# Performance work log

Measured on AMD Instinct MI355X. Metric: run time of the kernel, lower is better.

## Reference

```python
import jax, jax.numpy as jnp
import numpy as np

EPS = 1e-20
TEMP = 0.07
HEAD_DIM = 128


def setup_inputs() -> dict:
    key = jax.random.key(0)
    k1, k2, k3 = jax.random.split(key, 3)
    B, C, T, H, W = 4, 512, 8, 32, 32
    x = jax.random.normal(k1, (B, C, T, H, W), dtype=jnp.float32)
    W_head = jax.random.normal(k2, (C, HEAD_DIM), dtype=jnp.float32) / np.sqrt(C).astype(np.float32)
    b_head = jax.random.normal(k3, (HEAD_DIM,), dtype=jnp.float32) * 0.01
    return {"x": x, "W_head": W_head, "b_head": b_head}


def _forward(x, W_head, b_head):
    B, C, T, H, W = x.shape
    N = H * W
    # linear head over channel dim (equivalent to permute->Linear->permute)
    feats = jnp.einsum('bcthw,cd->bdthw', x, W_head) + b_head[None, :, None, None, None]
    keys = feats.reshape(B, HEAD_DIM, T, N)
    # F.normalize(p=2, dim=1): x / max(||x||, 1e-12)
    norm = jnp.maximum(jnp.linalg.norm(keys, axis=1, keepdims=True), 1e-12)
    keys = keys / norm
    # affinity between consecutive frames: [B, T-1, N, N]
    A = jnp.einsum('bctn,bctm->btnm', keys[:, :, :-1], keys[:, :, 1:])
    A12 = jax.nn.softmax(A / TEMP, axis=-1)                         # forward stochastic mats
    A21 = jax.nn.softmax(jnp.swapaxes(A, -1, -2) / TEMP, axis=-1)   # backward stochastic mats
    A12s = jnp.swapaxes(A12, 0, 1)  # [T-1, B, N, N]
    A21s = jnp.swapaxes(A21, 0, 1)  # [T-1, B, N, N]

    # prefix products P[i] = A12[0] @ A12[1] @ ... @ A12[i]
    def step_p(carry, a):
        c = carry @ a
        return c, c
    _, Ptail = jax.lax.scan(step_p, A12s[0], A12s[1:])
    P = jnp.concatenate([A12s[:1], Ptail], axis=0)  # [T-1, B, N, N]

    # suffix products S[i] = A21[i] @ A21[i-1] @ ... @ A21[0]
    def step_s(carry, a):
        c = a @ carry
        return c, c
    _, Stail = jax.lax.scan(step_s, A21s[0], A21s[1:])
    S = jnp.concatenate([A21s[:1], Stail], axis=0)  # [T-1, B, N, N]

    # cycle walks for i = 1..T-2: aar_i = P[i] @ S[i]
    aars = jnp.matmul(P[1:], S[1:])  # [T-2, B, N, N]
    logits = jnp.log(aars + EPS)
    # cross-entropy with identity targets: loss = logsumexp - logit[n, n]
    lse = jax.nn.logsumexp(logits, axis=-1)                  # [T-2, B, N]
    diag = jnp.diagonal(logits, axis1=-2, axis2=-1)          # [T-2, B, N]
    losses = jnp.mean(lse - diag, axis=(1, 2))               # [T-2]
    preds = jnp.argmax(logits, axis=-1)                      # [T-2, B, N]
    tgt = jnp.arange(N)[None, None, :]
    accs = jnp.mean((preds == tgt).astype(jnp.float32), axis=(1, 2))
    # original returns (loss_of_last_walk, diags); diags exposed as stacked arrays
    return losses[-1], losses, accs


def reference(x, W_head, b_head):
    return _forward(x, W_head, b_head)
```

## Files before the change

### kernel.cpp

```cpp
#include <hip/hip_runtime.h>
#include <cstdint>
#include <cstddef>

typedef unsigned short u16;
typedef unsigned long long u64;
using short8 = __attribute__((ext_vector_type(8))) short;
using f32x4  = __attribute__((ext_vector_type(4))) float;

#define KEXP 20.609929155556620f

__device__ __forceinline__ u16 f2bf(float f) {
  unsigned u = __float_as_uint(f);
  u += 0x7fffu + ((u >> 16) & 1u);
  return (u16)(u >> 16);
}
__device__ __forceinline__ float bf2f(u16 h) { return __uint_as_float(((unsigned)h) << 16); }

typedef const unsigned int GASu32 __attribute__((address_space(1)));
typedef unsigned int LASu32 __attribute__((address_space(3)));

__device__ __forceinline__ void gload16(const u16* src, u16* dstLds) {
  __builtin_amdgcn_global_load_lds((GASu32*)src, (LASu32*)dstLds, 16, 0, 0);
}

__global__ __launch_bounds__(256) void transpose_x(const float* __restrict__ x, u16* __restrict__ xT) {
  __shared__ float t[32][33];
  int b = blockIdx.z, c0 = blockIdx.y * 32, s0 = blockIdx.x * 32;
  int tid = threadIdx.x;
  int ci = tid >> 3, s4 = (tid & 7) * 4;
  float4 v = *(const float4*)(x + ((size_t)b * 512 + c0 + ci) * 8192 + s0 + s4);
  t[ci][s4 + 0] = v.x; t[ci][s4 + 1] = v.y; t[ci][s4 + 2] = v.z; t[ci][s4 + 3] = v.w;
  __syncthreads();
  int si = tid >> 3, c4 = (tid & 7) * 4;
  ushort4 o;
  o.x = f2bf(t[c4 + 0][si]); o.y = f2bf(t[c4 + 1][si]);
  o.z = f2bf(t[c4 + 2][si]); o.w = f2bf(t[c4 + 3][si]);
  *(ushort4*)(xT + ((size_t)b * 8192 + s0 + si) * 512 + c0 + c4) = o;
}

__global__ __launch_bounds__(256) void transpose_w(const float* __restrict__ W, u16* __restrict__ Wt) {
  int idx = blockIdx.x * 256 + threadIdx.x;
  int d = idx >> 9, c = idx & 511;
  Wt[idx] = (d < 128) ? f2bf(W[c * 128 + d]) : (u16)0;
}

__global__ __launch_bounds__(256) void normalize_keys(u16* __restrict__ keys) {
  int wv = threadIdx.x >> 6, lane = threadIdx.x & 63;
  int row = blockIdx.x * 4 + wv;
  unsigned* p = (unsigned*)(keys + (size_t)row * 128) + lane;
  unsigned v = *p;
  float a = bf2f((u16)(v & 0xffffu)), b = bf2f((u16)(v >> 16));
  float s = a * a + b * b;
  #pragma unroll
  for (int m = 1; m < 64; m <<= 1) s += __shfl_xor(s, m, 64);
  float sc = 1.f / fmaxf(sqrtf(s), 1e-12f);
  *p = (unsigned)f2bf(a * sc) | ((unsigned)f2bf(b * sc) << 16);
}

__global__ __launch_bounds__(256) void reduce_sums(const float* __restrict__ rsEP, const float* __restrict__ csEP,
                                                   float* __restrict__ rsumE, float* __restrict__ csumE) {
  int idx = blockIdx.x * 256 + threadIdx.x;
  if (idx < 28672) {
    int z = idx >> 10, r = idx & 1023;
    float s = 0.f;
    #pragma unroll
    for (int k = 0; k < 16; ++k) s += rsEP[(size_t)z * 16384 + k * 1024 + r];
    rsumE[z * 1024 + r] = s;
  } else {
    int b2 = idx - 28672;
    int z = b2 >> 10, c = b2 & 1023;
    float s = 0.f;
    #pragma unroll
    for (int k = 0; k < 8; ++k) s += csEP[(size_t)z * 8192 + k * 1024 + c];
    csumE[z * 1024 + c] = s;
  }
}

__global__ __launch_bounds__(256) void k3_t0(const u16* __restrict__ E, const float* __restrict__ rsum,
                                             const float* __restrict__ csum,
                                             u16* __restrict__ P0, u16* __restrict__ S0) {
  int b = blockIdx.z, r = blockIdx.x;
  int zE = b * 7;
  const u16* e = E + ((size_t)zE << 20) + (size_t)r * 1024;
  float rr = 1.f / rsum[zE * 1024 + r];
  int c = threadIdx.x * 4;
  ushort4 v = *(const ushort4*)(e + c);
  float4 cv = *(const float4*)(csum + zE * 1024 + c);
  ushort4 o1, o2;
  float v0 = bf2f(v.x), v1 = bf2f(v.y), v2 = bf2f(v.z), v3 = bf2f(v.w);
  o1.x = f2bf(v0 * rr); o1.y = f2bf(v1 * rr); o1.z = f2bf(v2 * rr); o1.w = f2bf(v3 * rr);
  o2.x = f2bf(v0 / cv.x); o2.y = f2bf(v1 / cv.y); o2.z = f2bf(v2 / cv.z); o2.w = f2bf(v3 / cv.w);
  size_t base = ((size_t)b << 20) + (size_t)r * 1024 + c;
  *(ushort4*)(P0 + base) = o1;
  *(ushort4*)(S0 + base) = o2;
}

__global__ __launch_bounds__(256) void k3_tr(const u16* __restrict__ E, const float* __restrict__ rsum,
                                             const float* __restrict__ csum,
                                             u16* __restrict__ Bp, u16* __restrict__ Bs) {
  __shared__ u16 t[64][66];
  int z = blockIdx.z; int b = z / 6, tt = z % 6 + 1;
  int zE = b * 7 + tt;
  int er0 = blockIdx.x * 64, ec0 = blockIdx.y * 64;
  const u16* e = E + ((size_t)zE << 20);
  int tid = threadIdx.x;
  int ri = tid >> 4, c4 = (tid & 15) * 4;
  #pragma unroll
  for (int p = 0; p < 4; ++p) {
    ushort4 v = *(const ushort4*)(e + (size_t)(er0 + ri + p * 16) * 1024 + ec0 + c4);
    t[ri + p * 16][c4 + 0] = v.x; t[ri + p * 16][c4 + 1] = v.y;
    t[ri + p * 16][c4 + 2] = v.z; t[ri + p * 16][c4 + 3] = v.w;
  }
  __syncthreads();
  size_t outBase = (size_t)(b * 6 + tt - 1) << 20;
  float ir0 = 1.f / rsum[zE * 1024 + er0 + c4 + 0];
  float ir1 = 1.f / rsum[zE * 1024 + er0 + c4 + 1];
  float ir2 = 1.f / rsum[zE * 1024 + er0 + c4 + 2];
  float ir3 = 1.f / rsum[zE * 1024 + er0 + c4 + 3];
  #pragma unroll
  for (int p = 0; p < 4; ++p) {
    int roL = ri + p * 16;
    int ro = ec0 + roL;
    float ic = 1.f / csum[zE * 1024 + ro];
    float v0 = bf2f(t[c4 + 0][roL]), v1 = bf2f(t[c4 + 1][roL]);
    float v2 = bf2f(t[c4 + 2][roL]), v3 = bf2f(t[c4 + 3][roL]);
    ushort4 op, os;
    op.x = f2bf(v0 * ir0); op.y = f2bf(v1 * ir1); op.z = f2bf(v2 * ir2); op.w = f2bf(v3 * ir3);
    os.x = f2bf(v0 * ic);  os.y = f2bf(v1 * ic);  os.z = f2bf(v2 * ic);  os.w = f2bf(v3 * ic);
    size_t off = outBase + (size_t)ro * 1024 + er0 + c4;
    *(ushort4*)(Bp + off) = op;
    *(ushort4*)(Bs + off) = os;
  }
}

struct GemmBatch { const u16* A[24]; const u16* B[24]; u16* C[8]; };
enum { M_HEAD = 0, M_EXP = 1, M_PLAIN = 2, M_AAR = 3 };

__device__ __forceinline__ int lds_off32(int r, int kbyte) {
  int rp = r >> 1;
  int sl = (((r & 1) << 2) | (kbyte >> 4)) ^ (rp & 7);
  return rp * 128 + sl * 16;
}

#define GEMM_BODY(T, FA, FB, NA, NB)                                                    \
  {                                                                                     \
    int t_ = (T);                                                                       \
    if (t_ + 1 < nt) {                                                                  \
      if (t_ + 2 < nt) asm volatile("s_waitcnt vmcnt(4)" ::: "memory");                 \
      else             asm volatile("s_waitcnt vmcnt(0)" ::: "memory");                 \
      __builtin_amdgcn_s_barrier();                                                     \
      __builtin_amdgcn_sched_barrier(0);                                                \
      _Pragma("unroll")                                                                 \
      for (int f = 0; f < 8; ++f) NA[f] = *(const short8*)((const char*)An + offA[f]);  \
      _Pragma("unroll")                                                                 \
      for (int f = 0; f < 4; ++f) NB[f] = *(const short8*)((const char*)Bn + offB[f]);  \
      if (t_ + 3 < nt) {                                                                \
        int k0_ = (t_ + 3) << 5;                                                        \
        gload16(sA0 + k0_, Ac + d0); gload16(sA1 + k0_, Ac + d1);                       \
        gload16(sB0 + k0_, Bc + d0); gload16(sB1 + k0_, Bc + d1);                       \
      }                                                                                 \
      asm volatile("s_waitcnt lgkmcnt(12)" ::: "memory");                               \
    } else {                                                                            \
      asm volatile("s_waitcnt lgkmcnt(0)" ::: "memory");                                \
    }                                                                                   \
    __builtin_amdgcn_sched_barrier(0);                                                  \
    __builtin_amdgcn_s_setprio(1);                                                      \
    _Pragma("unroll")                                                                   \
    for (int fa = 0; fa < 8; ++fa)                                                      \
      _Pragma("unroll")                                                                 \
      for (int fb = 0; fb < 4; ++fb)                                                    \
        acc[fa][fb] = __builtin_amdgcn_mfma_f32_16x16x32_bf16(FA[fa], FB[fb],           \
                                                              acc[fa][fb], 0, 0, 0);   \
    __builtin_amdgcn_s_setprio(0);                                                      \
    { u16* tA = Ac; Ac = An; An = A2; A2 = tA;                                          \
      u16* tB = Bc; Bc = Bn; Bn = B2; B2 = tB; }                                        \
  }

template <int MODE>
__global__ __launch_bounds__(512, 2) void gemm_nt(const u16* __restrict__ gA, const u16* __restrict__ gB,
                                                  u16* __restrict__ gC, GemmBatch batch,
                                                  const float* __restrict__ bias,
                                                  float* __restrict__ rsP, u64* __restrict__ amP,
                                                  float* __restrict__ diagv,
                                                  float* __restrict__ rsEP, float* __restrict__ csEP) {
  __shared__ u16 AsL[3][8192];
  __shared__ u16 BsL[3][8192];
  int tid = threadIdx.x, lane = tid & 63, wv = tid >> 6;
  int wrM = wv >> 2, wrN = wv & 3;
  int l15 = lane & 15, kb = (lane >> 4) << 4;

  int swz;
  { int per = (int)gridDim.x >> 3; int id0 = blockIdx.x; swz = (id0 & 7) * per + (id0 >> 3); }
  int z, m0, n0;
  if constexpr (MODE == M_HEAD) { z = 0; m0 = swz << 8; n0 = 0; }
  else { z = swz >> 4; int r4 = swz & 15; m0 = (r4 & 3) << 8; n0 = (r4 >> 2) << 8; }

  const u16 *A, *B; u16* C;
  int K, lda, ldb, ldc;
  if constexpr (MODE == M_HEAD) {
    A = gA; B = gB; C = gC; K = 512; lda = 512; ldb = 512; ldc = 128;
  } else if constexpr (MODE == M_EXP) {
    int b = z / 7, t = z % 7;
    size_t offA0 = (size_t)(b * 8 + t) * 131072;
    A = gA + offA0; B = gA + offA0 + 131072; C = gC + ((size_t)z << 20);
    K = 128; lda = 128; ldb = 128; ldc = 1024;
  } else if constexpr (MODE == M_PLAIN) {
    A = batch.A[z]; B = batch.B[z]; C = batch.C[z];
    K = 1024; lda = 1024; ldb = 1024; ldc = 1024;
  } else {
    A = batch.A[z]; B = batch.B[z]; C = nullptr;
    K = 1024; lda = 1024; ldb = 1024; ldc = 1024;
  }

  const u16 *sA0, *sA1, *sB0, *sB1;
  int d0 = tid * 8, d1 = (512 + tid) * 8;
  {
    int g0 = tid, g1 = 512 + tid;
    int rp0 = g0 >> 3, sp0 = (g0 & 7) ^ (rp0 & 7);
    int r0_ = (rp0 << 1) | (sp0 >> 2), kb0 = (sp0 & 3) * 8;
    int rp1 = g1 >> 3, sp1 = (g1 & 7) ^ (rp1 & 7);
    int r1_ = (rp1 << 1) | (sp1 >> 2), kb1 = (sp1 & 3) * 8;
    sA0 = A + (size_t)(m0 + r0_) * lda + kb0;
    sA1 = A + (size_t)(m0 + r1_) * lda + kb1;
    sB0 = B + (size_t)(n0 + r0_) * ldb + kb0;
    sB1 = B + (size_t)(n0 + r1_) * ldb + kb1;
  }
  int offA[8], offB[4];
  #pragma unroll
  for (int f = 0; f < 8; ++f) offA[f] = lds_off32(wrM * 128 + f * 16 + l15, kb);
  #pragma unroll
  for (int f = 0; f < 4; ++f) offB[f] = lds_off32(wrN * 64 + f * 16 + l15, kb);

  f32x4 acc[8][4] = {};
  int nt = K >> 5;

  u16 *Ac = AsL[0], *An = AsL[1], *A2 = AsL[2];
  u16 *Bc = BsL[0], *Bn = BsL[1], *B2 = BsL[2];

  gload16(sA0,      Ac + d0); gload16(sA1,      Ac + d1);
  gload16(sB0,      Bc + d0); gload16(sB1,      Bc + d1);
  gload16(sA0 + 32, An + d0); gload16(sA1 + 32, An + d1);
  gload16(sB0 + 32, Bn + d0); gload16(sB1 + 32, Bn + d1);
  gload16(sA0 + 64, A2 + d0); gload16(sA1 + 64, A2 + d1);
  gload16(sB0 + 64, B2 + d0); gload16(sB1 + 64, B2 + d1);
  asm volatile("s_waitcnt vmcnt(8)" ::: "memory");
  __builtin_amdgcn_s_barrier();
  __builtin_amdgcn_sched_barrier(0);
  short8 fa0[8], fb0[4], fa1[8], fb1[4];
  #pragma unroll
  for (int f = 0; f < 8; ++f) fa0[f] = *(const short8*)((const char*)Ac + offA[f]);
  #pragma unroll
  for (int f = 0; f < 4; ++f) fb0[f] = *(const short8*)((const char*)Bc + offB[f]);

  for (int t = 0; t < nt; t += 2) {
    GEMM_BODY(t,     fa0, fb0, fa1, fb1);
    GEMM_BODY(t + 1, fa1, fb1, fa0, fb0);
  }

  if constexpr (MODE == M_AAR) {
    int nb = n0 >> 8;
    size_t pbase = (size_t)z * 16384 + (size_t)((nb << 2) | wrN) * 1024;
    #pragma unroll
    for (int fa = 0; fa < 8; ++fa) {
      #pragma unroll
      for (int j = 0; j < 4; ++j) {
        float rs = 0.f, mv = -1.f; int mc = 0;
        #pragma unroll
        for (int fb = 0; fb < 4; ++fb) {
          float v = acc[fa][fb][j];
          rs += v;
          int c = n0 + (wrN << 6) + (fb << 4) + l15;
          if (v > mv) { mv = v; mc = c; }
        }
        u64 pk = ((u64)__float_as_uint(mv) << 32) | (u64)(unsigned)(1023 - mc);
        #pragma unroll
        for (int m = 1; m < 16; m <<= 1) {
          rs += __shfl_xor(rs, m, 64);
          u64 o = __shfl_xor(pk, m, 64);
          pk = (o > pk) ? o : pk;
        }
        if (l15 == 0) {
          int row = m0 + (wrM << 7) + (fa << 4) + ((lane >> 4) << 2) + j;
          rsP[pbase + row] = rs;
          amP[pbase + row] = pk;
        }
      }
      if (m0 == n0 && wrN == ((wrM << 1) | (fa >> 2))) {
        int fb = fa & 3;
        int jj = l15 - ((lane >> 4) << 2);
        if (jj >= 0 && jj < 4) {
          int row = m0 + (wrM << 7) + (fa << 4) + l15;
          float dv = (jj == 0) ? acc[fa][fb][0] : (jj == 1) ? acc[fa][fb][1]
                    : (jj == 2) ? acc[fa][fb][2] : acc[fa][fb][3];
          diagv[(z << 10) + row] = dv;
        }
      }
    }
  } else if constexpr (MODE == M_EXP) {
    float rp_[8][4] = {};
    float cp_[4] = {};
    #pragma unroll
    for (int fa = 0; fa < 8; ++fa)
      #pragma unroll
      for (int fb = 0; fb < 4; ++fb)
        #pragma unroll
        for (int j = 0; j < 4; ++j) {
          int row = m0 + (wrM << 7) + (fa << 4) + ((lane >> 4) << 2) + j;
          int col = n0 + (wrN << 6) + (fb << 4) + l15;
          float v = exp2f(acc[fa][fb][j] * KEXP);
          C[(size_t)row * ldc + col] = f2bf(v);
          rp_[fa][j] += v;
          cp_[fb] += v;
        }
    int nb = n0 >> 8, mb = m0 >> 8;
    size_t rbase = (size_t)z * 16384 + (size_t)((nb << 2) | wrN) * 1024;
    size_t cbase = (size_t)z * 8192 + (size_t)((mb << 1) | wrM) * 1024;
    #pragma unroll
    for (int fa = 0; fa < 8; ++fa)
      #pragma unroll
      for (int j = 0; j < 4; ++j) {
        float r = rp_[fa][j];
        r += __shfl_xor(r, 1, 64); r += __shfl_xor(r, 2, 64);
        r += __shfl_xor(r, 4, 64); r += __shfl_xor(r, 8, 64);
        if (l15 == 0) {
          int row = m0 + (wrM << 7) + (fa << 4) + ((lane >> 4) << 2) + j;
          rsEP[rbase + row] = r;
        }
      }
    #pragma unroll
    for (int fb = 0; fb < 4; ++fb) {
      float c = cp_[fb];
      c += __shfl_xor(c, 16, 64); c += __shfl_xor(c, 32, 64);
      if ((lane >> 4) == 0) {
        int col = n0 + (wrN << 6) + (fb << 4) + l15;
        csEP[cbase + col] = c;
      }
    }
  } else if constexpr (MODE == M_HEAD) {
    if (wrN < 2) {
      float bv[4][16 / 16];
      #pragma unroll
      for (int fb = 0; fb < 4; ++fb) bv[fb][0] = bias[(wrN << 6) + (fb << 4) + l15];
      #pragma unroll
      for (int fa = 0; fa < 8; ++fa)
        #pragma unroll
        for (int fb = 0; fb < 4; ++fb)
          #pragma unroll
          for (int j = 0; j < 4; ++j) {
            int row = m0 + (wrM << 7) + (fa << 4) + ((lane >> 4) << 2) + j;
            int col = (wrN << 6) + (fb << 4) + l15;
            C[(size_t)row * 128 + col] = f2bf(acc[fa][fb][j] + bv[fb][0]);
          }
    }
  } else {
    #pragma unroll
    for (int fa = 0; fa < 8; ++fa)
      #pragma unroll
      for (int fb = 0; fb < 4; ++fb)
        #pragma unroll
        for (int j = 0; j < 4; ++j) {
          int row = m0 + (wrM << 7) + (fa << 4) + ((lane >> 4) << 2) + j;
          int col = n0 + (wrN << 6) + (fb << 4) + l15;
          C[(size_t)row * 1024 + col] = f2bf(acc[fa][fb][j]);
        }
  }
}

__global__ __launch_bounds__(256) void finalize_k(const float* __restrict__ rsP, const u64* __restrict__ amP,
                                                  const float* __restrict__ diagv, float* __restrict__ out) {
  __shared__ float sl[256], sa[256];
  int w = blockIdx.x;
  int tid = threadIdx.x;
  float ls = 0.f, ac = 0.f;
  for (int idx = tid; idx < 4096; idx += 256) {
    int b = idx >> 10, n = idx & 1023;
    int z = (w << 2) + b;
    size_t base = (size_t)z * 16384 + n;
    float rs = 0.f; u64 pk = 0;
    #pragma unroll
    for (int k = 0; k < 16; ++k) {
      rs += rsP[base + k * 1024];
      u64 o = amP[base + k * 1024];
      pk = (o > pk) ? o : pk;
    }
    float dv = diagv[(z << 10) + n];
    ls += logf(rs + 1024.f * 1e-20f) - logf(dv + 1e-20f);
    unsigned pred = 1023u - (unsigned)(pk & 0xffffffffULL);
    ac += (pred == (unsigned)n) ? 1.f : 0.f;
  }
  sl[tid] = ls; sa[tid] = ac;
  __syncthreads();
  for (int s2 = 128; s2 > 0; s2 >>= 1) {
    if (tid < s2) { sl[tid] += sl[tid + s2]; sa[tid] += sa[tid + s2]; }
    __syncthreads();
  }
  if (tid == 0) {
    float loss = sl[0] / 4096.f, acv = sa[0] / 4096.f;
    out[1 + w] = loss;
    out[7 + w] = acv;
    if (w == 5) out[0] = loss;
  }
}

extern "C" void kernel_launch(void* const* d_in, const int* in_sizes, int n_in,
                              void* d_out, int out_size, void* d_ws, size_t ws_size,
                              hipStream_t stream) {
  (void)in_sizes; (void)n_in; (void)out_size; (void)ws_size;
  const float* x  = (const float*)d_in[0];
  const float* Wh = (const float*)d_in[1];
  const float* bh = (const float*)d_in[2];
  float* out = (float*)d_out;
  char* ws = (char*)d_ws;
  const size_t MB = 1ull << 20;

  u16* xT   = (u16*)(ws);
  u16* keys = (u16*)(ws + 32 * MB);
  float* rsP   = (float*)(ws + 32 * MB);
  u64*   amP   = (u64*)(ws + 34 * MB);
  float* diagv = (float*)(ws + 38 * MB);
  u16* WtP  = (u16*)(ws + 40 * MB);
  float* rsumE = (float*)(ws + 40 * MB + 288 * 1024);
  float* csumE = (float*)(ws + 40 * MB + 416 * 1024);
  u16* E    = (u16*)(ws + 41 * MB);
  float* rsEP  = (float*)(ws + 113 * MB);
  float* csEP  = (float*)(ws + 116 * MB);
  u16* Bp   = (u16*)(ws + 113 * MB);
  u16* Bs   = (u16*)(ws + 161 * MB);

  u16* Pb[7] = { (u16*)(ws + 97 * MB), (u16*)(ws + 0 * MB), (u16*)(ws + 8 * MB),
                 (u16*)(ws + 16 * MB), (u16*)(ws + 24 * MB), (u16*)(ws + 41 * MB),
                 (u16*)(ws + 49 * MB) };
  u16* Sb[7] = { (u16*)(ws + 105 * MB), (u16*)(ws + 57 * MB), (u16*)(ws + 65 * MB),
                 (u16*)(ws + 73 * MB), (u16*)(ws + 81 * MB), (u16*)(ws + 89 * MB),
                 (u16*)(ws + 97 * MB) };

  GemmBatch empty{};

  transpose_x<<<dim3(256, 16, 4), 256, 0, stream>>>(x, xT);
  transpose_w<<<dim3(512), 256, 0, stream>>>(Wh, WtP);
  gemm_nt<M_HEAD><<<dim3(128), 512, 0, stream>>>(xT, WtP, keys, empty, bh,
                                                 nullptr, nullptr, nullptr, nullptr, nullptr);
  normalize_keys<<<dim3(8192), 256, 0, stream>>>(keys);
  gemm_nt<M_EXP><<<dim3(448), 512, 0, stream>>>(keys, nullptr, E, empty, nullptr,
                                                nullptr, nullptr, nullptr, rsEP, csEP);
  reduce_sums<<<dim3(224), 256, 0, stream>>>(rsEP, csEP, rsumE, csumE);
  k3_t0<<<dim3(1024, 1, 4), 256, 0, stream>>>(E, rsumE, csumE, Pb[0], Sb[0]);
  k3_tr<<<dim3(16, 16, 24), 256, 0, stream>>>(E, rsumE, csumE, Bp, Bs);

  for (int i = 1; i <= 6; ++i) {
    GemmBatch gb{};
    for (int b = 0; b < 4; ++b) {
      gb.A[b]     = Pb[i - 1] + (size_t)b * 1048576;
      gb.B[b]     = Bp + (size_t)(b * 6 + i - 1) * 1048576;
      gb.C[b]     = Pb[i] + (size_t)b * 1048576;
      gb.A[4 + b] = Sb[i - 1] + (size_t)b * 1048576;
      gb.B[4 + b] = Bs + (size_t)(b * 6 + i - 1) * 1048576;
      gb.C[4 + b] = Sb[i] + (size_t)b * 1048576;
    }
    gemm_nt<M_PLAIN><<<dim3(128), 512, 0, stream>>>(nullptr, nullptr, nullptr, gb, nullptr,
                                                    nullptr, nullptr, nullptr, nullptr, nullptr);
  }

  GemmBatch ga{};
  for (int i = 1; i <= 6; ++i)
    for (int b = 0; b < 4; ++b) {
      ga.A[(i - 1) * 4 + b] = Pb[i] + (size_t)b * 1048576;
      ga.B[(i - 1) * 4 + b] = Sb[i] + (size_t)b * 1048576;
    }
  gemm_nt<M_AAR><<<dim3(384), 512, 0, stream>>>(nullptr, nullptr, nullptr, ga, nullptr,
                                                rsP, amP, diagv, nullptr, nullptr);
  finalize_k<<<dim3(6), 256, 0, stream>>>(rsP, amP, diagv, out);
}
```

Baseline: 387.2 us.

## Add 128x128 GEMM for chain products and restructure 256-tile pipeline

The six sequential prefix/suffix chain GEMMs now use a new 128x128-tile kernel with 256 threads and 512 blocks instead of 128 blocks of 256x256 tiles. This is meant to fill more CUs on the small dependent launches. The 256-tile kernel gets a 4-stage LDS ring with a prefetch distance of 2. Its inner loop now loads the A fragments in two halves with extra barriers, which lowers register pressure but adds synchronisation.

```diff
diff --git a/kernel.cpp b/kernel.cpp
--- a/kernel.cpp
+++ b/kernel.cpp
@@ -21,6 +21,15 @@
 
 __device__ __forceinline__ void gload16(const u16* src, u16* dstLds) {
   __builtin_amdgcn_global_load_lds((GASu32*)src, (LASu32*)dstLds, 16, 0, 0);
+}
+
+struct GemmBatch { const u16* A[24]; const u16* B[24]; u16* C[8]; };
+enum { M_HEAD = 0, M_EXP = 1, M_PLAIN = 2, M_AAR = 3 };
+
+__device__ __forceinline__ int lds_off32(int r, int kbyte) {
+  int rp = r >> 1;
+  int sl = (((r & 1) << 2) | (kbyte >> 4)) ^ (rp & 7);
+  return rp * 128 + sl * 16;
 }
 
 __global__ __launch_bounds__(256) void transpose_x(const float* __restrict__ x, u16* __restrict__ xT) {
@@ -133,16 +142,7 @@
   }
 }
 
-struct GemmBatch { const u16* A[24]; const u16* B[24]; u16* C[8]; };
-enum { M_HEAD = 0, M_EXP = 1, M_PLAIN = 2, M_AAR = 3 };
-
-__device__ __forceinline__ int lds_off32(int r, int kbyte) {
-  int rp = r >> 1;
-  int sl = (((r & 1) << 2) | (kbyte >> 4)) ^ (rp & 7);
-  return rp * 128 + sl * 16;
-}
-
-#define GEMM_BODY(T, FA, FB, NA, NB)                                                    \
+#define GB128(T, FA, FB, NA, NB)                                                        \
   {                                                                                     \
     int t_ = (T);                                                                       \
     if (t_ + 1 < nt) {                                                                  \
@@ -151,40 +151,120 @@
       __builtin_amdgcn_s_barrier();                                                     \
       __builtin_amdgcn_sched_barrier(0);                                                \
       _Pragma("unroll")                                                                 \
-      for (int f = 0; f < 8; ++f) NA[f] = *(const short8*)((const char*)An + offA[f]);  \
-      _Pragma("unroll")                                                                 \
-      for (int f = 0; f < 4; ++f) NB[f] = *(const short8*)((const char*)Bn + offB[f]);  \
+      for (int f = 0; f < 4; ++f) {                                                     \
+        NA[f] = *(const short8*)((const char*)An + offA[f]);                            \
+        NB[f] = *(const short8*)((const char*)Bn + offB[f]);                            \
+      }                                                                                 \
       if (t_ + 3 < nt) {                                                                \
         int k0_ = (t_ + 3) << 5;                                                        \
-        gload16(sA0 + k0_, Ac + d0); gload16(sA1 + k0_, Ac + d1);                       \
-        gload16(sB0 + k0_, Bc + d0); gload16(sB1 + k0_, Bc + d1);                       \
+        gload16(srcA0 + k0_, A3 + ldso0);                                               \
+        gload16(srcA1 + k0_, A3 + ldso1);                                               \
+        gload16(srcB0 + k0_, B3 + ldso0);                                               \
+        gload16(srcB1 + k0_, B3 + ldso1);                                               \
       }                                                                                 \
-      asm volatile("s_waitcnt lgkmcnt(12)" ::: "memory");                               \
+      asm volatile("s_waitcnt lgkmcnt(8)" ::: "memory");                                \
     } else {                                                                            \
       asm volatile("s_waitcnt lgkmcnt(0)" ::: "memory");                                \
     }                                                                                   \
     __builtin_amdgcn_sched_barrier(0);                                                  \
     __builtin_amdgcn_s_setprio(1);                                                      \
     _Pragma("unroll")                                                                   \
-    for (int fa = 0; fa < 8; ++fa)                                                      \
+    for (int fr = 0; fr < 4; ++fr)                                                      \
       _Pragma("unroll")                                                                 \
-      for (int fb = 0; fb < 4; ++fb)                                                    \
-        acc[fa][fb] = __builtin_amdgcn_mfma_f32_16x16x32_bf16(FA[fa], FB[fb],           \
-                                                              acc[fa][fb], 0, 0, 0);   \
+      for (int fc2 = 0; fc2 < 4; ++fc2)                                                 \
+        acc[fr][fc2] = __builtin_amdgcn_mfma_f32_16x16x32_bf16(FA[fr], FB[fc2],         \
+                                                               acc[fr][fc2], 0, 0, 0); \
     __builtin_amdgcn_s_setprio(0);                                                      \
-    { u16* tA = Ac; Ac = An; An = A2; A2 = tA;                                          \
-      u16* tB = Bc; Bc = Bn; Bn = B2; B2 = tB; }                                        \
-  }
+    { u16* tA = Ac; Ac = An; An = A2; A2 = A3; A3 = tA;                                 \
+      u16* tB = Bc; Bc = Bn; Bn = B2; B2 = B3; B3 = tB; }                               \
+  }
+
+__global__ __launch_bounds__(256) void gemm128(GemmBatch batch) {
+  __shared__ u16 AsL[4][4096];
+  __shared__ u16 BsL[4][4096];
+  int tid = threadIdx.x, lane = tid & 63, wv = tid >> 6;
+  int wr = wv >> 1, wc = wv & 1;
+  int l15 = lane & 15, kb = (lane >> 4) << 4;
+
+  int swz;
+  { int per = (int)gridDim.x >> 3; int id0 = blockIdx.x; swz = (id0 & 7) * per + (id0 >> 3); }
+  int z = swz >> 6; int r6 = swz & 63;
+  int m0 = (r6 & 7) << 7, n0 = (r6 >> 3) << 7;
+
+  const u16* A = batch.A[z];
+  const u16* B = batch.B[z];
+  u16* C = batch.C[z];
+  const int lda = 1024, ldb = 1024;
+  const int nt = 32;
+
+  const u16 *srcA0, *srcA1, *srcB0, *srcB1;
+  int ldso0, ldso1;
+  {
+    int g0 = tid, g1 = 256 + tid;
+    int rp0 = g0 >> 3, sp0 = (g0 & 7) ^ (rp0 & 7);
+    int r0_ = (rp0 << 1) | (sp0 >> 2), kb0 = (sp0 & 3) * 8;
+    int rp1 = g1 >> 3, sp1 = (g1 & 7) ^ (rp1 & 7);
+    int r1_ = (rp1 << 1) | (sp1 >> 2), kb1 = (sp1 & 3) * 8;
+    srcA0 = A + (size_t)(m0 + r0_) * lda + kb0;
+    srcA1 = A + (size_t)(m0 + r1_) * lda + kb1;
+    srcB0 = B + (size_t)(n0 + r0_) * ldb + kb0;
+    srcB1 = B + (size_t)(n0 + r1_) * ldb + kb1;
+    ldso0 = g0 * 8; ldso1 = g1 * 8;
+  }
+  int offA[4], offB[4];
+  #pragma unroll
+  for (int f = 0; f < 4; ++f) {
+    offA[f] = lds_off32((wr << 6) + (f << 4) + l15, kb);
+    offB[f] = lds_off32((wc << 6) + (f << 4) + l15, kb);
+  }
+
+  f32x4 acc[4][4] = {};
+
+  u16 *Ac = AsL[0], *An = AsL[1], *A2 = AsL[2], *A3 = AsL[3];
+  u16 *Bc = BsL[0], *Bn = BsL[1], *B2 = BsL[2], *B3 = BsL[3];
+
+  gload16(srcA0 +  0, Ac + ldso0); gload16(srcA1 +  0, Ac + ldso1);
+  gload16(srcB0 +  0, Bc + ldso0); gload16(srcB1 +  0, Bc + ldso1);
+  gload16(srcA0 + 32, An + ldso0); gload16(srcA1 + 32, An + ldso1);
+  gload16(srcB0 + 32, Bn + ldso0); gload16(srcB1 + 32, Bn + ldso1);
+  gload16(srcA0 + 64, A2 + ldso0); gload16(srcA1 + 64, A2 + ldso1);
+  gload16(srcB0 + 64, B2 + ldso0); gload16(srcB1 + 64, B2 + ldso1);
+  asm volatile("s_waitcnt vmcnt(8)" ::: "memory");
+  __builtin_amdgcn_s_barrier();
+  __builtin_amdgcn_sched_barrier(0);
+  short8 fa0[4], fb0[4], fa1[4], fb1[4];
+  #pragma unroll
+  for (int f = 0; f < 4; ++f) {
+    fa0[f] = *(const short8*)((const char*)Ac + offA[f]);
+    fb0[f] = *(const short8*)((const char*)Bc + offB[f]);
+  }
+
+  for (int t = 0; t < nt; t += 2) {
+    GB128(t,     fa0, fb0, fa1, fb1);
+    GB128(t + 1, fa1, fb1, fa0, fb0);
+  }
+
+  #pragma unroll
+  for (int fr = 0; fr < 4; ++fr)
+    #pragma unroll
+    for (int fc = 0; fc < 4; ++fc)
+      #pragma unroll
+      for (int j = 0; j < 4; ++j) {
+        int row = m0 + (wr << 6) + (fr << 4) + ((lane >> 4) << 2) + j;
+        int col = n0 + (wc << 6) + (fc << 4) + l15;
+        C[(size_t)row * 1024 + col] = f2bf(acc[fr][fc][j]);
+      }
+}
 
 template <int MODE>
-__global__ __launch_bounds__(512, 2) void gemm_nt(const u16* __restrict__ gA, const u16* __restrict__ gB,
+__global__ __launch_bounds__(512, 2) void gemm256(const u16* __restrict__ gA,
                                                   u16* __restrict__ gC, GemmBatch batch,
                                                   const float* __restrict__ bias,
                                                   float* __restrict__ rsP, u64* __restrict__ amP,
                                                   float* __restrict__ diagv,
                                                   float* __restrict__ rsEP, float* __restrict__ csEP) {
-  __shared__ u16 AsL[3][8192];
-  __shared__ u16 BsL[3][8192];
+  __shared__ u16 AsL[4][8192];
+  __shared__ u16 BsL[4][8192];
   int tid = threadIdx.x, lane = tid & 63, wv = tid >> 6;
   int wrM = wv >> 2, wrN = wv & 3;
   int l15 = lane & 15, kb = (lane >> 4) << 4;
@@ -198,15 +278,12 @@
   const u16 *A, *B; u16* C;
   int K, lda, ldb, ldc;
   if constexpr (MODE == M_HEAD) {
-    A = gA; B = gB; C = gC; K = 512; lda = 512; ldb = 512; ldc = 128;
+    A = gA; B = batch.B[0]; C = gC; K = 512; lda = 512; ldb = 512; ldc = 128;
   } else if constexpr (MODE == M_EXP) {
     int b = z / 7, t = z % 7;
     size_t offA0 = (size_t)(b * 8 + t) * 131072;
     A = gA + offA0; B = gA + offA0 + 131072; C = gC + ((size_t)z << 20);
     K = 128; lda = 128; ldb = 128; ldc = 1024;
-  } else if constexpr (MODE == M_PLAIN) {
-    A = batch.A[z]; B = batch.B[z]; C = batch.C[z];
-    K = 1024; lda = 1024; ldb = 1024; ldc = 1024;
   } else {
     A = batch.A[z]; B = batch.B[z]; C = nullptr;
     K = 1024; lda = 1024; ldb = 1024; ldc = 1024;
@@ -234,27 +311,57 @@
   f32x4 acc[8][4] = {};
   int nt = K >> 5;
 
-  u16 *Ac = AsL[0], *An = AsL[1], *A2 = AsL[2];
-  u16 *Bc = BsL[0], *Bn = BsL[1], *B2 = BsL[2];
-
-  gload16(sA0,      Ac + d0); gload16(sA1,      Ac + d1);
-  gload16(sB0,      Bc + d0); gload16(sB1,      Bc + d1);
-  gload16(sA0 + 32, An + d0); gload16(sA1 + 32, An + d1);
-  gload16(sB0 + 32, Bn + d0); gload16(sB1 + 32, Bn + d1);
-  gload16(sA0 + 64, A2 + d0); gload16(sA1 + 64, A2 + d1);
-  gload16(sB0 + 64, B2 + d0); gload16(sB1 + 64, B2 + d1);
-  asm volatile("s_waitcnt vmcnt(8)" ::: "memory");
+  gload16(sA0,      AsL[0] + d0); gload16(sA1,      AsL[0] + d1);
+  gload16(sB0,      BsL[0] + d0); gload16(sB1,      BsL[0] + d1);
+  gload16(sA0 + 32, AsL[1] + d0); gload16(sA1 + 32, AsL[1] + d1);
+  gload16(sB0 + 32, BsL[1] + d0); gload16(sB1 + 32, BsL[1] + d1);
+  asm volatile("s_waitcnt vmcnt(4)" ::: "memory");
   __builtin_amdgcn_s_barrier();
-  __builtin_amdgcn_sched_barrier(0);
-  short8 fa0[8], fb0[4], fa1[8], fb1[4];
-  #pragma unroll
-  for (int f = 0; f < 8; ++f) fa0[f] = *(const short8*)((const char*)Ac + offA[f]);
-  #pragma unroll
-  for (int f = 0; f < 4; ++f) fb0[f] = *(const short8*)((const char*)Bc + offB[f]);
-
-  for (int t = 0; t < nt; t += 2) {
-    GEMM_BODY(t,     fa0, fb0, fa1, fb1);
-    GEMM_BODY(t + 1, fa1, fb1, fa0, fb0);
+
+  for (int t = 0; t < nt; ++t) {
+    const u16* At = AsL[t & 3];
+    const u16* Bt = BsL[t & 3];
+    u16* Ad = AsL[(t + 2) & 3];
+    u16* Bd = BsL[(t + 2) & 3];
+    int k2 = (t + 2) << 5;
+    bool st = (t + 2) < nt;
+    short8 aF[4], bF[4];
+    #pragma unroll
+    for (int f = 0; f < 4; ++f) bF[f] = *(const short8*)((const char*)Bt + offB[f]);
+    #pragma unroll
+    for (int f = 0; f < 4; ++f) aF[f] = *(const short8*)((const char*)At + offA[f]);
+    if (st) { gload16(sA0 + k2, Ad + d0); gload16(sA1 + k2, Ad + d1); }
+    __builtin_amdgcn_sched_barrier(0);
+    __builtin_amdgcn_s_barrier();
+    asm volatile("s_waitcnt lgkmcnt(0)" ::: "memory");
+    __builtin_amdgcn_sched_barrier(0);
+    __builtin_amdgcn_s_setprio(1);
+    #pragma unroll
+    for (int fa = 0; fa < 4; ++fa)
+      #pragma unroll
+      for (int fb = 0; fb < 4; ++fb)
+        acc[fa][fb] = __builtin_amdgcn_mfma_f32_16x16x32_bf16(aF[fa], bF[fb], acc[fa][fb], 0, 0, 0);
+    __builtin_amdgcn_s_setprio(0);
+    __builtin_amdgcn_sched_barrier(0);
+    __builtin_amdgcn_s_barrier();
+    #pragma unroll
+    for (int f = 0; f < 4; ++f) aF[f] = *(const short8*)((const char*)At + offA[4 + f]);
+    if (st) { gload16(sB0 + k2, Bd + d0); gload16(sB1 + k2, Bd + d1); }
+    if (st) asm volatile("s_waitcnt vmcnt(4)" ::: "memory");
+    else    asm volatile("s_waitcnt vmcnt(0)" ::: "memory");
+    __builtin_amdgcn_sched_barrier(0);
+    __builtin_amdgcn_s_barrier();
+    asm volatile("s_waitcnt lgkmcnt(0)" ::: "memory");
+    __builtin_amdgcn_sched_barrier(0);
+    __builtin_amdgcn_s_setprio(1);
+    #pragma unroll
+    for (int fa = 0; fa < 4; ++fa)
+      #pragma unroll
+      for (int fb = 0; fb < 4; ++fb)
+        acc[4 + fa][fb] = __builtin_amdgcn_mfma_f32_16x16x32_bf16(aF[fa], bF[fb], acc[4 + fa][fb], 0, 0, 0);
+    __builtin_amdgcn_s_setprio(0);
+    __builtin_amdgcn_sched_barrier(0);
+    __builtin_amdgcn_s_barrier();
   }
 
   if constexpr (MODE == M_AAR) {
@@ -336,11 +443,11 @@
         csEP[cbase + col] = c;
       }
     }
-  } else if constexpr (MODE == M_HEAD) {
+  } else {
     if (wrN < 2) {
-      float bv[4][16 / 16];
-      #pragma unroll
-      for (int fb = 0; fb < 4; ++fb) bv[fb][0] = bias[(wrN << 6) + (fb << 4) + l15];
+      float bv[4];
+      #pragma unroll
+      for (int fb = 0; fb < 4; ++fb) bv[fb] = bias[(wrN << 6) + (fb << 4) + l15];
       #pragma unroll
       for (int fa = 0; fa < 8; ++fa)
         #pragma unroll
@@ -349,20 +456,9 @@
           for (int j = 0; j < 4; ++j) {
             int row = m0 + (wrM << 7) + (fa << 4) + ((lane >> 4) << 2) + j;
             int col = (wrN << 6) + (fb << 4) + l15;
-            C[(size_t)row * 128 + col] = f2bf(acc[fa][fb][j] + bv[fb][0]);
+            C[(size_t)row * 128 + col] = f2bf(acc[fa][fb][j] + bv[fb]);
           }
     }
-  } else {
-    #pragma unroll
-    for (int fa = 0; fa < 8; ++fa)
-      #pragma unroll
-      for (int fb = 0; fb < 4; ++fb)
-        #pragma unroll
-        for (int j = 0; j < 4; ++j) {
-          int row = m0 + (wrM << 7) + (fa << 4) + ((lane >> 4) << 2) + j;
-          int col = n0 + (wrN << 6) + (fb << 4) + l15;
-          C[(size_t)row * 1024 + col] = f2bf(acc[fa][fb][j]);
-        }
   }
 }
 
@@ -438,10 +534,13 @@
 
   transpose_x<<<dim3(256, 16, 4), 256, 0, stream>>>(x, xT);
   transpose_w<<<dim3(512), 256, 0, stream>>>(Wh, WtP);
-  gemm_nt<M_HEAD><<<dim3(128), 512, 0, stream>>>(xT, WtP, keys, empty, bh,
-                                                 nullptr, nullptr, nullptr, nullptr, nullptr);
+  {
+    GemmBatch hb{}; hb.B[0] = WtP;
+    gemm256<M_HEAD><<<dim3(128), 512, 0, stream>>>(xT, keys, hb, bh,
+                                                   nullptr, nullptr, nullptr, nullptr, nullptr);
+  }
   normalize_keys<<<dim3(8192), 256, 0, stream>>>(keys);
-  gemm_nt<M_EXP><<<dim3(448), 512, 0, stream>>>(keys, nullptr, E, empty, nullptr,
+  gemm256<M_EXP><<<dim3(448), 512, 0, stream>>>(keys, E, empty, nullptr,
                                                 nullptr, nullptr, nullptr, rsEP, csEP);
   reduce_sums<<<dim3(224), 256, 0, stream>>>(rsEP, csEP, rsumE, csumE);
   k3_t0<<<dim3(1024, 1, 4), 256, 0, stream>>>(E, rsumE, csumE, Pb[0], Sb[0]);
@@ -457,8 +556,7 @@
       gb.B[4 + b] = Bs + (size_t)(b * 6 + i - 1) * 1048576;
       gb.C[4 + b] = Sb[i] + (size_t)b * 1048576;
     }
-    gemm_nt<M_PLAIN><<<dim3(128), 512, 0, stream>>>(nullptr, nullptr, nullptr, gb, nullptr,
-                                                    nullptr, nullptr, nullptr, nullptr, nullptr);
+    gemm128<<<dim3(512), 256, 0, stream>>>(gb);
   }
 
   GemmBatch ga{};
@@ -467,7 +565,7 @@
       ga.A[(i - 1) * 4 + b] = Pb[i] + (size_t)b * 1048576;
       ga.B[(i - 1) * 4 + b] = Sb[i] + (size_t)b * 1048576;
     }
-  gemm_nt<M_AAR><<<dim3(384), 512, 0, stream>>>(nullptr, nullptr, nullptr, ga, nullptr,
+  gemm256<M_AAR><<<dim3(384), 512, 0, stream>>>(nullptr, nullptr, ga, nullptr,
                                                 rsP, amP, diagv, nullptr, nullptr);
   finalize_k<<<dim3(6), 256, 0, stream>>>(rsP, amP, diagv, out);
 }
```

New measurement: 337.5 us. -12.8%, faster.
